# Optimization experiments

Measured on AMD Instinct MI355X. Metric: run time of the kernel, lower is better.

The kernel has to match this reference:

```python
import jax, jax.numpy as jnp
import numpy as np

N_NODES = 100000
N_EDGES = 1600000
NODE_NF = 11   # num_node_fs
EDGE_NF = 4    # edges_nf
H_NF = 128     # h_nf
EMB_NF = 4     # emb_nf


def _linear_params(k, fan_in, fan_out):
    # torch nn.Linear default init: U(-1/sqrt(fan_in), 1/sqrt(fan_in))
    lim = 1.0 / np.sqrt(fan_in)
    kw, kb = jax.random.split(k)
    W = jax.random.uniform(kw, (fan_in, fan_out), minval=-lim, maxval=lim, dtype=jnp.float32)
    b = jax.random.uniform(kb, (fan_out,), minval=-lim, maxval=lim, dtype=jnp.float32)
    return W, b


def setup_inputs() -> dict:
    key = jax.random.key(0)
    ks = jax.random.split(key, 8)
    node_feats = jax.random.normal(ks[0], (N_NODES, NODE_NF), dtype=jnp.float32)
    edge_index = jax.random.randint(ks[1], (2, N_EDGES), 0, N_NODES, dtype=jnp.int32)
    edge_attr = jax.random.normal(ks[2], (N_EDGES, EDGE_NF), dtype=jnp.float32)
    # NELayer edge MLP: Linear(2*in_nf+edges_nf, h_nf) -> ReLU -> Linear(h_nf, h_nf) -> ReLU
    eW1, eb1 = _linear_params(ks[3], 2 * NODE_NF + EDGE_NF, H_NF)
    eW2, eb2 = _linear_params(ks[4], H_NF, H_NF)
    # NELayer node MLP: Linear(in_nf+h_nf, h_nf) -> ReLU -> Linear(h_nf, out_nf=h_nf)
    nW1, nb1 = _linear_params(ks[5], NODE_NF + H_NF, H_NF)
    nW2, nb2 = _linear_params(ks[6], H_NF, H_NF)
    # fc_emb: Linear(h_nf, emb_nf)
    fW, fb = _linear_params(ks[7], H_NF, EMB_NF)
    return dict(node_feats=node_feats, edge_index=edge_index, edge_attr=edge_attr,
                eW1=eW1, eb1=eb1, eW2=eW2, eb2=eb2,
                nW1=nW1, nb1=nb1, nW2=nW2, nb2=nb2, fW=fW, fb=fb)


def reference(node_feats, edge_index, edge_attr,
              eW1, eb1, eW2, eb2, nW1, nb1, nW2, nb2, fW, fb):
    row, col = edge_index[0], edge_index[1]          # [E], [E]
    src = node_feats[row]                            # [E, NODE_NF] gather
    dst = node_feats[col]                            # [E, NODE_NF] gather
    # edge model
    e_in = jnp.concatenate([src, dst, edge_attr], axis=1)   # [E, 2*NODE_NF+EDGE_NF]
    e_h = jax.nn.relu(e_in @ eW1 + eb1)
    edge_feats = jax.nn.relu(e_h @ eW2 + eb2)                # [E, H_NF]
    # node model: scatter-sum edge feats to source nodes
    agg = jax.ops.segment_sum(edge_feats, row, num_segments=node_feats.shape[0])  # [N, H_NF]
    n_in = jnp.concatenate([node_feats, agg], axis=1)        # [N, NODE_NF+H_NF]
    n_h = jax.nn.relu(n_in @ nW1 + nb1)
    h = n_h @ nW2 + nb2                                      # [N, H_NF]
    # embedding head
    return h @ fW + fb                                       # [N, EMB_NF]
```

## Files before the change

kernel.cpp:

```cpp
#include <hip/hip_runtime.h>

#define N_NODES 100000
#define N_EDGES 1600000
#define NODE_NF 11
#define EDGE_NF 4
#define H_NF 128
#define SCAN_B 1024
#define NBLK ((N_NODES + SCAN_B - 1) / SCAN_B)

#define K1P 40
#define K2P 136
#define EFP 131
#define K1N 160

typedef _Float16 half8 __attribute__((ext_vector_type(8)));
typedef float floatx4 __attribute__((ext_vector_type(4)));

__device__ inline half8 load8f(const float* p) {
    float4 x0 = *(const float4*)(p);
    float4 x1 = *(const float4*)(p + 4);
    half8 r;
    r[0]=(_Float16)x0.x; r[1]=(_Float16)x0.y; r[2]=(_Float16)x0.z; r[3]=(_Float16)x0.w;
    r[4]=(_Float16)x1.x; r[5]=(_Float16)x1.y; r[6]=(_Float16)x1.z; r[7]=(_Float16)x1.w;
    return r;
}
__device__ inline half8 zero8() {
    half8 z;
    #pragma unroll
    for (int j = 0; j < 8; ++j) z[j] = (_Float16)0.f;
    return z;
}

#define SEG0 (N_NODES * 12)
#define SEG1 (SEG0 + H_NF * K1P)
#define SEG2 (SEG1 + H_NF * K2P)
#define SEG3 (SEG2 + H_NF * K1N)
#define SEG4 (SEG3 + 16 * K2P + 4)
#define SEG5 (SEG4 + N_EDGES)

__global__ __launch_bounds__(256)
void prep_hist_kernel(const float* __restrict__ nf,
                      const float* __restrict__ eW1,
                      const float* __restrict__ eb1,
                      const float* __restrict__ eW2,
                      const float* __restrict__ nW1,
                      const float* __restrict__ nW2,
                      const float* __restrict__ fW,
                      const float* __restrict__ nb2,
                      const float* __restrict__ fb,
                      const int*   __restrict__ edge_index,
                      _Float16* __restrict__ nfh,
                      _Float16* __restrict__ w1h,
                      _Float16* __restrict__ w2h,
                      _Float16* __restrict__ w1nh,
                      _Float16* __restrict__ w23h,
                      float* __restrict__ b23,
                      int* hist)
{
    int i = blockIdx.x * 256 + threadIdx.x;
    if (i < SEG0) {
        int n = i / 12, k = i - n * 12;
        nfh[i] = (k < NODE_NF) ? (_Float16)nf[(size_t)n * NODE_NF + k] : (_Float16)0.f;
    } else if (i < SEG1) {
        int j = i - SEG0;
        int n = j / K1P, k = j - n * K1P;
        float v = 0.f;
        if (k < 11)                 v = eW1[k * H_NF + n];
        else if (k >= 12 && k < 23) v = eW1[(k - 1) * H_NF + n];
        else if (k >= 24 && k < 28) v = eW1[(k - 2) * H_NF + n];
        else if (k == 28)           v = eb1[n];
        w1h[j] = (_Float16)v;
    } else if (i < SEG2) {
        int j = i - SEG1;
        int n = j / K2P, k = j - n * K2P;
        float v = 0.f;
        if (k < H_NF) {
            int ks = k >> 5, rem = k & 31, q = rem >> 3, jj = rem & 7;
            int ka = ks * 32 + ((jj >> 2) << 4) + q * 4 + (jj & 3);
            v = eW2[ka * H_NF + n];
        }
        w2h[j] = (_Float16)v;
    } else if (i < SEG3) {
        int j = i - SEG2;
        int n = j / K1N, k = j - n * K1N;
        float v = 0.f;
        if (k < 11)                  v = nW1[k * H_NF + n];
        else if (k >= 12 && k < 140) v = nW1[(k - 1) * H_NF + n];
        w1nh[j] = (_Float16)v;
    } else if (i < SEG4) {
        int j = i - SEG3;
        if (j < 16 * K2P) {
            int n = j / K2P, k = j - n * K2P;
            float v = 0.f;
            if (n < 4 && k < H_NF) {
                for (int q = 0; q < H_NF; ++q) v += nW2[k * H_NF + q] * fW[q * 4 + n];
            }
            w23h[j] = (_Float16)v;
        } else {
            int o = j - 16 * K2P;
            float v = fb[o];
            for (int q = 0; q < H_NF; ++q) v += nb2[q] * fW[q * 4 + o];
            b23[o] = v;
        }
    } else if (i < SEG5) {
        int e = i - SEG4;
        atomicAdd(&hist[edge_index[e]], 1);
    }
}

__global__ __launch_bounds__(256)
void transpose_w2(const float* __restrict__ W, float* __restrict__ WT) {
    int i = blockIdx.x * 256 + threadIdx.x;
    if (i < H_NF * H_NF) {
        int k = i >> 7, j = i & (H_NF - 1);
        WT[j * H_NF + k] = W[i];
    }
}

__global__ __launch_bounds__(SCAN_B)
void scan1_kernel(const int* __restrict__ hist, int* starts, int* bsum) {
    __shared__ int buf[SCAN_B];
    int i = blockIdx.x * SCAN_B + threadIdx.x;
    int v = (i < N_NODES) ? hist[i] : 0;
    buf[threadIdx.x] = v;
    __syncthreads();
    for (int off = 1; off < SCAN_B; off <<= 1) {
        int t = (threadIdx.x >= off) ? buf[threadIdx.x - off] : 0;
        __syncthreads();
        buf[threadIdx.x] += t;
        __syncthreads();
    }
    if (i < N_NODES) starts[i] = buf[threadIdx.x] - v;
    if (threadIdx.x == SCAN_B - 1) bsum[blockIdx.x] = buf[SCAN_B - 1];
}

__global__ void scan2_kernel(int* bsum) {
    if (threadIdx.x == 0 && blockIdx.x == 0) {
        int run = 0;
        for (int b = 0; b < NBLK; ++b) { int t = bsum[b]; bsum[b] = run; run += t; }
        bsum[NBLK] = run;
    }
}

__global__ __launch_bounds__(256)
void scan3_kernel(int* starts, int* cursor, const int* __restrict__ bsum) {
    int i = blockIdx.x * 256 + threadIdx.x;
    if (i < N_NODES) {
        int s = starts[i] + bsum[i / SCAN_B];
        starts[i] = s;
        cursor[i] = s;
    }
    if (i == 0) starts[N_NODES] = bsum[NBLK];
}

__global__ __launch_bounds__(256)
void permrec_kernel(const int* __restrict__ edge_index,
                    const float* __restrict__ edge_attr,
                    int* cursor,
                    int4* __restrict__ rec)
{
    int e = blockIdx.x * 256 + threadIdx.x;
    if (e >= N_EDGES) return;
    int row = edge_index[e];
    int col = edge_index[N_EDGES + e];
    float4 a4 = ((const float4*)edge_attr)[e];
    union { _Float16 h[4]; int2 v; } u;
    u.h[0] = (_Float16)a4.x; u.h[1] = (_Float16)a4.y;
    u.h[2] = (_Float16)a4.z; u.h[3] = (_Float16)a4.w;
    int pos = atomicAdd(&cursor[row], 1);
    rec[pos] = make_int4(row, col, u.v.x, u.v.y);
}

__global__ __launch_bounds__(256)
void permute_kernel(const int* __restrict__ edge_index, int* cursor, int* perm) {
    int e = blockIdx.x * 256 + threadIdx.x;
    if (e < N_EDGES) {
        int pos = atomicAdd(&cursor[edge_index[e]], 1);
        perm[pos] = e;
    }
}

__global__ __launch_bounds__(256, 2)
void edge_mfma_kernel(const int4* __restrict__ recs,
                      const _Float16* __restrict__ nfh,
                      const _Float16* __restrict__ w1h,
                      const _Float16* __restrict__ w2h,
                      const float* __restrict__ eb2,
                      float* agg)
{
    int t = threadIdx.x;
    int wv = t >> 6, lane = t & 63;
    int m = lane & 15, quad = lane >> 4;

    half8 w1f[8], w2f[8][4];
    #pragma unroll
    for (int tile = 0; tile < 8; ++tile)
        w1f[tile] = *(const half8*)(w1h + (tile * 16 + m) * K1P + quad * 8);
    #pragma unroll
    for (int tile = 0; tile < 8; ++tile)
        #pragma unroll
        for (int ks = 0; ks < 4; ++ks)
            w2f[tile][ks] = *(const half8*)(w2h + (tile * 16 + m) * K2P + ks * 32 + quad * 8);
    float b2v[8];
    #pragma unroll
    for (int tile = 0; tile < 8; ++tile)
        b2v[tile] = eb2[tile * 16 + m];

    const int nwin = N_EDGES / 16;
    const int STRIDE = gridDim.x * 4;
    int win = blockIdx.x * 4 + wv;
    if (win >= nwin) return;

    int4 rc = recs[win * 16 + m];
    int2 g0 = make_int2(0, 0), g1 = g0, g2 = g0;
    if (quad < 2) {
        int node = (quad == 0) ? rc.x : rc.y;
        const int2* p = (const int2*)(nfh + (size_t)node * 12);
        g0 = p[0]; g1 = p[1]; g2 = p[2];
    }

    while (true) {
        int next = win + STRIDE;
        bool hn = next < nwin;
        int4 rcn = make_int4(0, 0, 0, 0);
        if (hn) rcn = recs[next * 16 + m];

        int sAx = __shfl(g2.x, m),      sAy = __shfl(g2.y, m);
        int sBx = __shfl(g1.x, m + 16), sBy = __shfl(g1.y, m + 16);
        int sCx = __shfl(g2.x, m + 16), sCy = __shfl(g2.y, m + 16);
        int d0 = (quad == 0) ? g0.x : (quad == 1) ? sAx : (quad == 2) ? sBx : rc.z;
        int d1 = (quad == 0) ? g0.y : (quad == 1) ? sAy : (quad == 2) ? sBy : rc.w;
        int d2 = (quad == 0) ? g1.x : (quad == 1) ? g0.x : (quad == 2) ? sCx : 0x00003C00;
        int d3 = (quad == 0) ? g1.y : (quad == 1) ? g0.y : (quad == 2) ? sCy : 0;
        union { int i[4]; half8 h; } ua;
        ua.i[0] = d0; ua.i[1] = d1; ua.i[2] = d2; ua.i[3] = d3;
        half8 a1 = ua.h;

        union { unsigned u[4]; half8 h; } ua2[4];
        #pragma unroll
        for (int tile = 0; tile < 8; ++tile) {
            floatx4 c = {0.f, 0.f, 0.f, 0.f};
            c = __builtin_amdgcn_mfma_f32_16x16x32_f16(w1f[tile], a1, c, 0, 0, 0);
            union { _Float16 f[2]; unsigned u; } p0, p1;
            p0.f[0] = (_Float16)fmaxf(c[0], 0.f);
            p0.f[1] = (_Float16)fmaxf(c[1], 0.f);
            p1.f[0] = (_Float16)fmaxf(c[2], 0.f);
            p1.f[1] = (_Float16)fmaxf(c[3], 0.f);
            ua2[tile >> 1].u[(tile & 1) * 2 + 0] = p0.u;
            ua2[tile >> 1].u[(tile & 1) * 2 + 1] = p1.u;
        }

        float vals[32];
        #pragma unroll
        for (int tile = 0; tile < 8; ++tile) {
            floatx4 c = {0.f, 0.f, 0.f, 0.f};
            #pragma unroll
            for (int ks = 0; ks < 4; ++ks)
                c = __builtin_amdgcn_mfma_f32_16x16x32_f16(ua2[ks].h, w2f[tile][ks], c, 0, 0, 0);
            #pragma unroll
            for (int r = 0; r < 4; ++r)
                vals[tile * 4 + r] = fmaxf(c[r] + b2v[tile], 0.f);
        }

        int2 n0 = make_int2(0, 0), n1 = n0, n2 = n0;
        if (hn && quad < 2) {
            int node = (quad == 0) ? rcn.x : rcn.y;
            const int2* p = (const int2*)(nfh + (size_t)node * 12);
            n0 = p[0]; n1 = p[1]; n2 = p[2];
        }

        int row = rc.x;
        int rprev = __shfl(row, lane - 1);
        bool bi = (lane < 16) && (m == 0 || rprev != row);
        unsigned long long bm = __ballot(bi);
        unsigned mk = (unsigned)(bm & 0xFFFFull);
        int er0 = __shfl(row, quad * 4 + 0);
        int er1 = __shfl(row, quad * 4 + 1);
        int er2 = __shfl(row, quad * 4 + 2);
        int er3 = __shfl(row, quad * 4 + 3);
        while (mk) {
            int start = __builtin_ctz(mk);
            mk &= mk - 1;
            int srow = __shfl(row, start);
            float s[8];
            #pragma unroll
            for (int tile = 0; tile < 8; ++tile) {
                float v = 0.f;
                if (er0 == srow) v += vals[tile * 4 + 0];
                if (er1 == srow) v += vals[tile * 4 + 1];
                if (er2 == srow) v += vals[tile * 4 + 2];
                if (er3 == srow) v += vals[tile * 4 + 3];
                s[tile] = v;
            }
            #pragma unroll
            for (int tile = 0; tile < 8; ++tile) {
                s[tile] += __shfl_xor(s[tile], 16);
                s[tile] += __shfl_xor(s[tile], 32);
            }
            if (quad == 0) {
                #pragma unroll
                for (int tile = 0; tile < 8; ++tile)
                    unsafeAtomicAdd(&agg[(size_t)srow * H_NF + tile * 16 + m], s[tile]);
            }
        }

        if (!hn) break;
        win = next; rc = rcn; g0 = n0; g1 = n1; g2 = n2;
    }
}

#define G_W1      0
#define G_W2      10240
#define G_ARENA   45056
#define G_ARENA_SZ 8448
#define G_TOTAL   (G_ARENA + 4 * G_ARENA_SZ)

__global__ __launch_bounds__(256, 2)
void edge_mfma_gather_kernel(const _Float16* __restrict__ nfh,
                             const int*   __restrict__ edge_index,
                             const float* __restrict__ edge_attr,
                             const _Float16* __restrict__ w1h,
                             const float* __restrict__ eb1,
                             const _Float16* __restrict__ w2h,
                             const float* __restrict__ eb2,
                             const int*   __restrict__ perm,
                             float* agg)
{
    __shared__ __align__(16) char smem[G_TOTAL];
    _Float16* W1s = (_Float16*)(smem + G_W1);
    _Float16* W2s = (_Float16*)(smem + G_W2);
    int t = threadIdx.x;
    {
        const float4* g1 = (const float4*)w1h;
        float4* s1 = (float4*)W1s;
        for (int i = t; i < 640; i += 256) s1[i] = g1[i];
        const float4* g2 = (const float4*)w2h;
        float4* s2 = (float4*)W2s;
        for (int i = t; i < 2176; i += 256) s2[i] = g2[i];
    }
    __syncthreads();

    int wv = t >> 6, lane = t & 63;
    char* arena = smem + G_ARENA + wv * G_ARENA_SZ;
    _Float16* Ain  = (_Float16*)arena;
    _Float16* Hs   = (_Float16*)(arena + 1280);
    float*    efS  = (float*)arena;
    int*      rowsS = (int*)(arena + 8384);

    int m = lane & 15, quad = lane >> 4;
    int el = lane & 15, grp = lane >> 4;
    _Float16* arow = Ain + el * K1P;

    float b1v[8], b2v[8];
    #pragma unroll
    for (int tile = 0; tile < 8; ++tile) {
        b1v[tile] = eb1[tile * 16 + m];
        b2v[tile] = eb2[tile * 16 + m];
    }

    const int nwin = N_EDGES / 16;
    for (int win = blockIdx.x * 4 + wv; win < nwin; win += gridDim.x * 4) {
        int e = perm[win * 16 + el];
        if (grp < 2) {
            int node = edge_index[grp * N_EDGES + e];
            const int2* p = (const int2*)(nfh + (size_t)node * 12);
            int2 x0 = p[0], x1 = p[1], x2 = p[2];
            char* dst = (char*)(arow + grp * 12);
            *(int2*)(dst) = x0; *(int2*)(dst + 8) = x1; *(int2*)(dst + 16) = x2;
        } else if (grp == 2) {
            float4 a4 = ((const float4*)edge_attr)[e];
            arow[24] = (_Float16)a4.x; arow[25] = (_Float16)a4.y;
            arow[26] = (_Float16)a4.z; arow[27] = (_Float16)a4.w;
        } else {
            rowsS[el] = edge_index[e];
            *(int2*)((char*)arow + 56) = make_int2(0, 0);
        }

        half8 a1 = *(const half8*)(Ain + m * K1P + quad * 8);
        #pragma unroll
        for (int tile = 0; tile < 8; ++tile) {
            half8 b = *(const half8*)(W1s + (tile * 16 + m) * K1P + quad * 8);
            floatx4 c = {0.f, 0.f, 0.f, 0.f};
            c = __builtin_amdgcn_mfma_f32_16x16x32_f16(a1, b, c, 0, 0, 0);
            int n = tile * 16 + m;
            #pragma unroll
            for (int r = 0; r < 4; ++r)
                Hs[(quad * 4 + r) * K2P + n] = (_Float16)fmaxf(c[r] + b1v[tile], 0.f);
        }
        half8 a2[4];
        #pragma unroll
        for (int ks = 0; ks < 4; ++ks) {
            const _Float16* hp = Hs + m * K2P + ks * 32 + quad * 4;
            union { int2 d[2]; half8 h; } uu;
            uu.d[0] = *(const int2*)(hp);
            uu.d[1] = *(const int2*)(hp + 16);
            a2[ks] = uu.h;
        }
        #pragma unroll
        for (int tile = 0; tile < 8; ++tile) {
            floatx4 c = {0.f, 0.f, 0.f, 0.f};
            #pragma unroll
            for (int ks = 0; ks < 4; ++ks) {
                half8 b = *(const half8*)(W2s + (tile * 16 + m) * K2P + ks * 32 + quad * 8);
                c = __builtin_amdgcn_mfma_f32_16x16x32_f16(a2[ks], b, c, 0, 0, 0);
            }
            #pragma unroll
            for (int r = 0; r < 4; ++r)
                efS[(quad * 4 + r) * EFP + tile * 16 + m] = fmaxf(c[r] + b2v[tile], 0.f);
        }

        int f = lane;
        int cur = rowsS[0];
        float acc0 = efS[f], acc1 = efS[64 + f];
        #pragma unroll 1
        for (int i = 1; i < 16; ++i) {
            int r = rowsS[i];
            float v0 = efS[i * EFP + f];
            float v1 = efS[i * EFP + 64 + f];
            if (r != cur) {
                unsafeAtomicAdd(&agg[(size_t)cur * H_NF + f], acc0);
                unsafeAtomicAdd(&agg[(size_t)cur * H_NF + 64 + f], acc1);
                acc0 = v0; acc1 = v1; cur = r;
            } else { acc0 += v0; acc1 += v1; }
        }
        unsafeAtomicAdd(&agg[(size_t)cur * H_NF + f], acc0);
        unsafeAtomicAdd(&agg[(size_t)cur * H_NF + 64 + f], acc1);
    }
}

#define N_W1    0
#define N_W23   40960
#define N_HS    45312

__global__ __launch_bounds__(256, 2)
void node_mfma_kernel(const float* __restrict__ node_feats,
                      const float* __restrict__ agg,
                      const _Float16* __restrict__ w1nh,
                      const float* __restrict__ nb1,
                      const _Float16* __restrict__ w23h,
                      const float* __restrict__ b23,
                      float* __restrict__ out)
{
    __shared__ __align__(16) char smem[N_HS + 4 * 4352];
    _Float16* W1N  = (_Float16*)(smem + N_W1);
    _Float16* W23s = (_Float16*)(smem + N_W23);
    int t = threadIdx.x;
    {
        const float4* g1 = (const float4*)w1nh;
        float4* s1 = (float4*)W1N;
        for (int i = t; i < 2560; i += 256) s1[i] = g1[i];
        const float4* g2 = (const float4*)w23h;
        float4* s2 = (float4*)W23s;
        for (int i = t; i < 272; i += 256) s2[i] = g2[i];
    }
    __syncthreads();

    int wv = t >> 6, lane = t & 63;
    int m = lane & 15, quad = lane >> 4;
    _Float16* HsW = (_Float16*)(smem + N_HS + wv * 4352);
    const int ntile = (N_NODES + 63) / 64;

    float nb1v[8];
    #pragma unroll
    for (int tile = 0; tile < 8; ++tile) nb1v[tile] = nb1[tile * 16 + m];
    float b23v = (m < 4) ? b23[m] : 0.f;

    for (int ti = blockIdx.x; ti < ntile; ti += gridDim.x) {
        int nb = (ti * 4 + wv) * 16;
        if (nb >= N_NODES) continue;
        int nodeA = nb + m;
        if (nodeA >= N_NODES) nodeA = N_NODES - 1;
        const float* ag  = agg + (size_t)nodeA * H_NF;
        const float* nfp = node_feats + (size_t)nodeA * NODE_NF;

        half8 afr[5];
        if (quad == 0) {
            half8 r;
            #pragma unroll
            for (int j = 0; j < 8; ++j) r[j] = (_Float16)nfp[j];
            afr[0] = r;
            afr[4] = load8f(ag + 116);
        } else if (quad == 1) {
            half8 r;
            r[0] = (_Float16)nfp[8]; r[1] = (_Float16)nfp[9];
            r[2] = (_Float16)nfp[10]; r[3] = (_Float16)0.f;
            float4 x = *(const float4*)(ag);
            r[4] = (_Float16)x.x; r[5] = (_Float16)x.y;
            r[6] = (_Float16)x.z; r[7] = (_Float16)x.w;
            afr[0] = r;
            float4 y = *(const float4*)(ag + 124);
            half8 s = zero8();
            s[0] = (_Float16)y.x; s[1] = (_Float16)y.y;
            s[2] = (_Float16)y.z; s[3] = (_Float16)y.w;
            afr[4] = s;
        } else if (quad == 2) {
            afr[0] = load8f(ag + 4);
            afr[4] = zero8();
        } else {
            afr[0] = load8f(ag + 12);
            afr[4] = zero8();
        }
        afr[1] = load8f(ag + 20 + 8 * quad);
        afr[2] = load8f(ag + 52 + 8 * quad);
        afr[3] = load8f(ag + 84 + 8 * quad);

        #pragma unroll
        for (int tile = 0; tile < 8; ++tile) {
            floatx4 c = {0.f, 0.f, 0.f, 0.f};
            #pragma unroll
            for (int ks = 0; ks < 5; ++ks) {
                half8 b = *(const half8*)(W1N + (tile * 16 + m) * K1N + ks * 32 + quad * 8);
                c = __builtin_amdgcn_mfma_f32_16x16x32_f16(afr[ks], b, c, 0, 0, 0);
            }
            #pragma unroll
            for (int r = 0; r < 4; ++r)
                HsW[(quad * 4 + r) * K2P + tile * 16 + m] = (_Float16)fmaxf(c[r] + nb1v[tile], 0.f);
        }

        half8 a2[4];
        #pragma unroll
        for (int ks = 0; ks < 4; ++ks)
            a2[ks] = *(const half8*)(HsW + m * K2P + ks * 32 + quad * 8);
        floatx4 c23 = {0.f, 0.f, 0.f, 0.f};
        #pragma unroll
        for (int ks = 0; ks < 4; ++ks) {
            half8 b = *(const half8*)(W23s + m * K2P + ks * 32 + quad * 8);
            c23 = __builtin_amdgcn_mfma_f32_16x16x32_f16(a2[ks], b, c23, 0, 0, 0);
        }
        if (m < 4) {
            #pragma unroll
            for (int r = 0; r < 4; ++r) {
                int node = nb + quad * 4 + r;
                if (node < N_NODES) out[node * 4 + m] = c23[r] + b23v;
            }
        }
    }
}

__global__ __launch_bounds__(256)
void edge_kernel_atomic(const float* __restrict__ node_feats,
                        const int*   __restrict__ edge_index,
                        const float* __restrict__ edge_attr,
                        const float* __restrict__ eW1,
                        const float* __restrict__ eb1,
                        const float* __restrict__ W2T,
                        const float* __restrict__ eb2,
                        float* agg)
{
    int e = blockIdx.x * 256 + threadIdx.x;
    if (e >= N_EDGES) return;
    int row = edge_index[e];
    int col = edge_index[N_EDGES + e];
    float h[H_NF];
    #pragma unroll
    for (int j = 0; j < H_NF; ++j) h[j] = eb1[j];
    const float* srcp = node_feats + (size_t)row * NODE_NF;
    #pragma unroll 1
    for (int k = 0; k < NODE_NF; ++k) {
        float x = srcp[k];
        const float* w = eW1 + k * H_NF;
        #pragma unroll
        for (int j = 0; j < H_NF; ++j) h[j] = fmaf(x, w[j], h[j]);
    }
    const float* dstp = node_feats + (size_t)col * NODE_NF;
    #pragma unroll 1
    for (int k = 0; k < NODE_NF; ++k) {
        float x = dstp[k];
        const float* w = eW1 + (NODE_NF + k) * H_NF;
        #pragma unroll
        for (int j = 0; j < H_NF; ++j) h[j] = fmaf(x, w[j], h[j]);
    }
    float4 at = ((const float4*)edge_attr)[e];
    float av[EDGE_NF] = {at.x, at.y, at.z, at.w};
    #pragma unroll
    for (int k = 0; k < EDGE_NF; ++k) {
        float x = av[k];
        const float* w = eW1 + (2 * NODE_NF + k) * H_NF;
        #pragma unroll
        for (int j = 0; j < H_NF; ++j) h[j] = fmaf(x, w[j], h[j]);
    }
    #pragma unroll
    for (int j = 0; j < H_NF; ++j) h[j] = fmaxf(h[j], 0.f);
    #pragma unroll 1
    for (int j0 = 0; j0 < H_NF; j0 += 8) {
        float acc[8];
        #pragma unroll
        for (int jj = 0; jj < 8; ++jj) acc[jj] = eb2[j0 + jj];
        #pragma unroll
        for (int k = 0; k < H_NF; ++k) {
            float x = h[k];
            #pragma unroll
            for (int jj = 0; jj < 8; ++jj)
                acc[jj] = fmaf(x, W2T[(j0 + jj) * H_NF + k], acc[jj]);
        }
        #pragma unroll
        for (int jj = 0; jj < 8; ++jj)
            unsafeAtomicAdd(&agg[(size_t)row * H_NF + j0 + jj], fmaxf(acc[jj], 0.f));
    }
}

__global__ __launch_bounds__(256)
void node_kernel1(const float* __restrict__ node_feats, float* agg_nh,
                  const float* __restrict__ nW1, const float* __restrict__ nb1)
{
    int n = blockIdx.x * 256 + threadIdx.x;
    if (n >= N_NODES) return;
    float acc[H_NF];
    #pragma unroll
    for (int j = 0; j < H_NF; ++j) acc[j] = nb1[j];
    const float* nfp = node_feats + (size_t)n * NODE_NF;
    #pragma unroll 1
    for (int k = 0; k < NODE_NF; ++k) {
        float x = nfp[k];
        const float* w = nW1 + k * H_NF;
        #pragma unroll
        for (int j = 0; j < H_NF; ++j) acc[j] = fmaf(x, w[j], acc[j]);
    }
    const float4* ap = (const float4*)(agg_nh + (size_t)n * H_NF);
    #pragma unroll 1
    for (int k4 = 0; k4 < H_NF / 4; ++k4) {
        float4 x = ap[k4];
        const float* w0 = nW1 + (NODE_NF + k4 * 4 + 0) * H_NF;
        const float* w1 = nW1 + (NODE_NF + k4 * 4 + 1) * H_NF;
        const float* w2 = nW1 + (NODE_NF + k4 * 4 + 2) * H_NF;
        const float* w3 = nW1 + (NODE_NF + k4 * 4 + 3) * H_NF;
        #pragma unroll
        for (int j = 0; j < H_NF; ++j) {
            acc[j] = fmaf(x.x, w0[j], acc[j]);
            acc[j] = fmaf(x.y, w1[j], acc[j]);
            acc[j] = fmaf(x.z, w2[j], acc[j]);
            acc[j] = fmaf(x.w, w3[j], acc[j]);
        }
    }
    float* op = agg_nh + (size_t)n * H_NF;
    #pragma unroll
    for (int j4 = 0; j4 < H_NF / 4; ++j4) {
        float4 o = make_float4(fmaxf(acc[j4*4+0], 0.f), fmaxf(acc[j4*4+1], 0.f),
                               fmaxf(acc[j4*4+2], 0.f), fmaxf(acc[j4*4+3], 0.f));
        ((float4*)op)[j4] = o;
    }
}

__global__ __launch_bounds__(256)
void node_kernel2(const float* __restrict__ nh, const float* __restrict__ nW2,
                  const float* __restrict__ nb2, const float* __restrict__ fW,
                  const float* __restrict__ fb, float* __restrict__ out)
{
    int n = blockIdx.x * 256 + threadIdx.x;
    if (n >= N_NODES) return;
    float acc[H_NF];
    #pragma unroll
    for (int j = 0; j < H_NF; ++j) acc[j] = nb2[j];
    const float4* hp = (const float4*)(nh + (size_t)n * H_NF);
    #pragma unroll 1
    for (int k4 = 0; k4 < H_NF / 4; ++k4) {
        float4 x = hp[k4];
        const float* w0 = nW2 + (k4 * 4 + 0) * H_NF;
        const float* w1 = nW2 + (k4 * 4 + 1) * H_NF;
        const float* w2 = nW2 + (k4 * 4 + 2) * H_NF;
        const float* w3 = nW2 + (k4 * 4 + 3) * H_NF;
        #pragma unroll
        for (int j = 0; j < H_NF; ++j) {
            acc[j] = fmaf(x.x, w0[j], acc[j]);
            acc[j] = fmaf(x.y, w1[j], acc[j]);
            acc[j] = fmaf(x.z, w2[j], acc[j]);
            acc[j] = fmaf(x.w, w3[j], acc[j]);
        }
    }
    float o0 = fb[0], o1 = fb[1], o2 = fb[2], o3 = fb[3];
    #pragma unroll
    for (int j = 0; j < H_NF; ++j) {
        o0 = fmaf(acc[j], fW[j * 4 + 0], o0);
        o1 = fmaf(acc[j], fW[j * 4 + 1], o1);
        o2 = fmaf(acc[j], fW[j * 4 + 2], o2);
        o3 = fmaf(acc[j], fW[j * 4 + 3], o3);
    }
    ((float4*)out)[n] = make_float4(o0, o1, o2, o3);
}

extern "C" void kernel_launch(void* const* d_in, const int* in_sizes, int n_in,
                              void* d_out, int out_size, void* d_ws, size_t ws_size,
                              hipStream_t stream)
{
    const float* node_feats = (const float*)d_in[0];
    const int*   edge_index = (const int*)d_in[1];
    const float* edge_attr  = (const float*)d_in[2];
    const float* eW1 = (const float*)d_in[3];
    const float* eb1 = (const float*)d_in[4];
    const float* eW2 = (const float*)d_in[5];
    const float* eb2 = (const float*)d_in[6];
    const float* nW1 = (const float*)d_in[7];
    const float* nb1 = (const float*)d_in[8];
    const float* nW2 = (const float*)d_in[9];
    const float* nb2 = (const float*)d_in[10];
    const float* fW  = (const float*)d_in[11];
    const float* fb  = (const float*)d_in[12];
    float* out = (float*)d_out;

    size_t off = 0;
    auto carve = [&](size_t bytes) {
        void* p = (char*)d_ws + off;
        off = (off + bytes + 255) & ~(size_t)255;
        return p;
    };
    float*     agg    = (float*)carve((size_t)N_NODES * H_NF * sizeof(float));
    int*       hist   = (int*)  carve((size_t)N_NODES * sizeof(int));
    size_t zero_bytes = off;
    int*       starts = (int*)  carve((size_t)(N_NODES + 1) * sizeof(int));
    int*       cursor = (int*)  carve((size_t)N_NODES * sizeof(int));
    int*       bsum   = (int*)  carve((size_t)(NBLK + 1) * sizeof(int));
    _Float16*  nfh    = (_Float16*)carve((size_t)N_NODES * 12 * sizeof(_Float16));
    _Float16*  w1h    = (_Float16*)carve((size_t)H_NF * K1P * sizeof(_Float16));
    _Float16*  w2h    = (_Float16*)carve((size_t)H_NF * K2P * sizeof(_Float16));
    _Float16*  w1nh   = (_Float16*)carve((size_t)H_NF * K1N * sizeof(_Float16));
    _Float16*  w23h   = (_Float16*)carve((size_t)16 * K2P * sizeof(_Float16));
    float*     b23    = (float*)carve(4 * sizeof(float));
    int*       perm   = (int*)  carve((size_t)N_EDGES * sizeof(int));
    size_t required_t2 = off;
    int4*      rec    = (int4*) carve((size_t)N_EDGES * sizeof(int4));
    size_t required_t1 = off;

    if (ws_size >= required_t2) {
        hipMemsetAsync(d_ws, 0, zero_bytes, stream);
        prep_hist_kernel<<<(SEG5 + 255) / 256, 256, 0, stream>>>(
            node_feats, eW1, eb1, eW2, nW1, nW2, fW, nb2, fb, edge_index,
            nfh, w1h, w2h, w1nh, w23h, b23, hist);
        scan1_kernel<<<NBLK, SCAN_B, 0, stream>>>(hist, starts, bsum);
        scan2_kernel<<<1, 64, 0, stream>>>(bsum);
        scan3_kernel<<<(N_NODES + 255) / 256, 256, 0, stream>>>(starts, cursor, bsum);

        if (ws_size >= required_t1) {
            permrec_kernel<<<(N_EDGES + 255) / 256, 256, 0, stream>>>(
                edge_index, edge_attr, cursor, rec);
            edge_mfma_kernel<<<512, 256, 0, stream>>>(
                rec, nfh, w1h, w2h, eb2, agg);
        } else {
            permute_kernel<<<(N_EDGES + 255) / 256, 256, 0, stream>>>(edge_index, cursor, perm);
            edge_mfma_gather_kernel<<<512, 256, 0, stream>>>(
                nfh, edge_index, edge_attr, w1h, eb1, w2h, eb2, perm, agg);
        }
        node_mfma_kernel<<<512, 256, 0, stream>>>(
            node_feats, agg, w1nh, nb1, w23h, b23, out);
    } else {
        float* agg_fb = (float*)d_ws;
        float* W2T_fb = (float*)((char*)d_ws + (size_t)N_NODES * H_NF * sizeof(float));
        transpose_w2<<<(H_NF * H_NF + 255) / 256, 256, 0, stream>>>(eW2, W2T_fb);
        hipMemsetAsync(agg_fb, 0, (size_t)N_NODES * H_NF * sizeof(float), stream);
        edge_kernel_atomic<<<(N_EDGES + 255) / 256, 256, 0, stream>>>(
            node_feats, edge_index, edge_attr, eW1, eb1, W2T_fb, eb2, agg_fb);
        node_kernel1<<<(N_NODES + 255) / 256, 256, 0, stream>>>(node_feats, agg_fb, nW1, nb1);
        node_kernel2<<<(N_NODES + 255) / 256, 256, 0, stream>>>(agg_fb, nW2, nb2, fW, fb, out);
    }
}
```

Baseline: 412.5 us.

## Keep node MLP hidden in registers, fold bias into GEMM, parallelize block scan

The node kernel now swaps MFMA operands so the first-layer output lands in a register layout that feeds the second MFMA directly, removing the per-wave LDS staging buffer. To make that work, the W23 weights are permuted to match. The nb1 bias is folded into the weight matrix through a constant-one input column. The single-thread block-sum scan becomes a 128-thread shared-memory scan, and the node kernel grid grows from 512 to 768 blocks, which the smaller LDS footprint allows.

```diff
diff --git a/kernel.cpp b/kernel.cpp
--- a/kernel.cpp
+++ b/kernel.cpp
@@ -44,6 +44,7 @@
                       const float* __restrict__ eb1,
                       const float* __restrict__ eW2,
                       const float* __restrict__ nW1,
+                      const float* __restrict__ nb1,
                       const float* __restrict__ nW2,
                       const float* __restrict__ fW,
                       const float* __restrict__ nb2,
@@ -86,6 +87,7 @@
         float v = 0.f;
         if (k < 11)                  v = nW1[k * H_NF + n];
         else if (k >= 12 && k < 140) v = nW1[(k - 1) * H_NF + n];
+        else if (k == 140)           v = nb1[n];
         w1nh[j] = (_Float16)v;
     } else if (i < SEG4) {
         int j = i - SEG3;
@@ -93,7 +95,10 @@
             int n = j / K2P, k = j - n * K2P;
             float v = 0.f;
             if (n < 4 && k < H_NF) {
-                for (int q = 0; q < H_NF; ++q) v += nW2[k * H_NF + q] * fW[q * 4 + n];
+                int ks = k >> 5, rem = k & 31, q = rem >> 3, jj = rem & 7;
+                int ka = ks * 32 + ((jj >> 2) << 4) + q * 4 + (jj & 3);
+                for (int q2 = 0; q2 < H_NF; ++q2)
+                    v += nW2[ka * H_NF + q2] * fW[q2 * 4 + n];
             }
             w23h[j] = (_Float16)v;
         } else {
@@ -134,12 +139,21 @@
     if (threadIdx.x == SCAN_B - 1) bsum[blockIdx.x] = buf[SCAN_B - 1];
 }
 
-__global__ void scan2_kernel(int* bsum) {
-    if (threadIdx.x == 0 && blockIdx.x == 0) {
-        int run = 0;
-        for (int b = 0; b < NBLK; ++b) { int t = bsum[b]; bsum[b] = run; run += t; }
-        bsum[NBLK] = run;
-    }
+__global__ __launch_bounds__(128)
+void scan2_kernel(int* bsum) {
+    __shared__ int buf[128];
+    int i = threadIdx.x;
+    int v = (i < NBLK) ? bsum[i] : 0;
+    buf[i] = v;
+    __syncthreads();
+    for (int off = 1; off < 128; off <<= 1) {
+        int t = (i >= off) ? buf[i - off] : 0;
+        __syncthreads();
+        buf[i] += t;
+        __syncthreads();
+    }
+    if (i < NBLK) bsum[i] = buf[i] - v;
+    if (i == NBLK - 1) bsum[NBLK] = buf[i];
 }
 
 __global__ __launch_bounds__(256)
@@ -430,18 +444,17 @@
 
 #define N_W1    0
 #define N_W23   40960
-#define N_HS    45312
+#define N_TOTAL 45312
 
 __global__ __launch_bounds__(256, 2)
 void node_mfma_kernel(const float* __restrict__ node_feats,
                       const float* __restrict__ agg,
                       const _Float16* __restrict__ w1nh,
-                      const float* __restrict__ nb1,
                       const _Float16* __restrict__ w23h,
                       const float* __restrict__ b23,
                       float* __restrict__ out)
 {
-    __shared__ __align__(16) char smem[N_HS + 4 * 4352];
+    __shared__ __align__(16) char smem[N_TOTAL];
     _Float16* W1N  = (_Float16*)(smem + N_W1);
     _Float16* W23s = (_Float16*)(smem + N_W23);
     int t = threadIdx.x;
@@ -457,12 +470,8 @@
 
     int wv = t >> 6, lane = t & 63;
     int m = lane & 15, quad = lane >> 4;
-    _Float16* HsW = (_Float16*)(smem + N_HS + wv * 4352);
     const int ntile = (N_NODES + 63) / 64;
 
-    float nb1v[8];
-    #pragma unroll
-    for (int tile = 0; tile < 8; ++tile) nb1v[tile] = nb1[tile * 16 + m];
     float b23v = (m < 4) ? b23[m] : 0.f;
 
     for (int ti = blockIdx.x; ti < ntile; ti += gridDim.x) {
@@ -492,6 +501,7 @@
             half8 s = zero8();
             s[0] = (_Float16)y.x; s[1] = (_Float16)y.y;
             s[2] = (_Float16)y.z; s[3] = (_Float16)y.w;
+            s[4] = (_Float16)1.f;
             afr[4] = s;
         } else if (quad == 2) {
             afr[0] = load8f(ag + 4);
@@ -504,28 +514,29 @@
         afr[2] = load8f(ag + 52 + 8 * quad);
         afr[3] = load8f(ag + 84 + 8 * quad);
 
+        union { unsigned u[4]; half8 h; } ua2[4];
         #pragma unroll
         for (int tile = 0; tile < 8; ++tile) {
             floatx4 c = {0.f, 0.f, 0.f, 0.f};
             #pragma unroll
             for (int ks = 0; ks < 5; ++ks) {
-                half8 b = *(const half8*)(W1N + (tile * 16 + m) * K1N + ks * 32 + quad * 8);
-                c = __builtin_amdgcn_mfma_f32_16x16x32_f16(afr[ks], b, c, 0, 0, 0);
+                half8 wfr = *(const half8*)(W1N + (tile * 16 + m) * K1N + ks * 32 + quad * 8);
+                c = __builtin_amdgcn_mfma_f32_16x16x32_f16(wfr, afr[ks], c, 0, 0, 0);
             }
-            #pragma unroll
-            for (int r = 0; r < 4; ++r)
-                HsW[(quad * 4 + r) * K2P + tile * 16 + m] = (_Float16)fmaxf(c[r] + nb1v[tile], 0.f);
-        }
-
-        half8 a2[4];
-        #pragma unroll
-        for (int ks = 0; ks < 4; ++ks)
-            a2[ks] = *(const half8*)(HsW + m * K2P + ks * 32 + quad * 8);
+            union { _Float16 f[2]; unsigned u; } p0, p1;
+            p0.f[0] = (_Float16)fmaxf(c[0], 0.f);
+            p0.f[1] = (_Float16)fmaxf(c[1], 0.f);
+            p1.f[0] = (_Float16)fmaxf(c[2], 0.f);
+            p1.f[1] = (_Float16)fmaxf(c[3], 0.f);
+            ua2[tile >> 1].u[(tile & 1) * 2 + 0] = p0.u;
+            ua2[tile >> 1].u[(tile & 1) * 2 + 1] = p1.u;
+        }
+
         floatx4 c23 = {0.f, 0.f, 0.f, 0.f};
         #pragma unroll
         for (int ks = 0; ks < 4; ++ks) {
             half8 b = *(const half8*)(W23s + m * K2P + ks * 32 + quad * 8);
-            c23 = __builtin_amdgcn_mfma_f32_16x16x32_f16(a2[ks], b, c23, 0, 0, 0);
+            c23 = __builtin_amdgcn_mfma_f32_16x16x32_f16(ua2[ks].h, b, c23, 0, 0, 0);
         }
         if (m < 4) {
             #pragma unroll
@@ -723,10 +734,10 @@
     if (ws_size >= required_t2) {
         hipMemsetAsync(d_ws, 0, zero_bytes, stream);
         prep_hist_kernel<<<(SEG5 + 255) / 256, 256, 0, stream>>>(
-            node_feats, eW1, eb1, eW2, nW1, nW2, fW, nb2, fb, edge_index,
+            node_feats, eW1, eb1, eW2, nW1, nb1, nW2, fW, nb2, fb, edge_index,
             nfh, w1h, w2h, w1nh, w23h, b23, hist);
         scan1_kernel<<<NBLK, SCAN_B, 0, stream>>>(hist, starts, bsum);
-        scan2_kernel<<<1, 64, 0, stream>>>(bsum);
+        scan2_kernel<<<1, 128, 0, stream>>>(bsum);
         scan3_kernel<<<(N_NODES + 255) / 256, 256, 0, stream>>>(starts, cursor, bsum);
 
         if (ws_size >= required_t1) {
@@ -739,8 +750,8 @@
             edge_mfma_gather_kernel<<<512, 256, 0, stream>>>(
                 nfh, edge_index, edge_attr, w1h, eb1, w2h, eb2, perm, agg);
         }
-        node_mfma_kernel<<<512, 256, 0, stream>>>(
-            node_feats, agg, w1nh, nb1, w23h, b23, out);
+        node_mfma_kernel<<<768, 256, 0, stream>>>(
+            node_feats, agg, w1nh, w23h, b23, out);
     } else {
         float* agg_fb = (float*)d_ws;
         float* W2T_fb = (float*)((char*)d_ws + (size_t)N_NODES * H_NF * sizeof(float));
```

Measured after the change: 415.7 us. No clear change (+0.8%).
